# Optimization experiments

Hardware: AMD Instinct MI355X
Metric: run time of the kernel (lower is better)

The kernel has to match this reference:

```python
import jax, jax.numpy as jnp
import numpy as np

N, E = 50000, 800000
NODE_DIM, EDGE_DIM = 128, 32
EGO_H, PEER_H, EDGE_H = 64, 64, 32  # node_hidden=128 split; edge_hidden=32


def setup_inputs() -> dict:
    key = jax.random.key(0)
    ks = jax.random.split(key, 9)
    x = jax.random.normal(ks[0], (N, NODE_DIM), dtype=jnp.float32)
    edge_attrs = jax.random.normal(ks[1], (E, EDGE_DIM), dtype=jnp.float32)
    edge_index = jax.random.randint(ks[2], (2, E), 0, N, dtype=jnp.int32)
    # Linear params (torch convention: W [out, in]), num_layers=1 -> single emb Linear per MLPLayer
    def lin(k, out_d, in_d):
        kw, kb = jax.random.split(k)
        s = 1.0 / np.sqrt(in_d)
        return (jax.random.uniform(kw, (out_d, in_d), minval=-s, maxval=s, dtype=jnp.float32),
                jax.random.uniform(kb, (out_d,), minval=-s, maxval=s, dtype=jnp.float32))
    W_peer, b_peer = lin(ks[3], PEER_H + EDGE_H, NODE_DIM + EDGE_DIM)
    W_ego, b_ego = lin(ks[4], EGO_H, NODE_DIM)
    W_edge, b_edge = lin(ks[5], EDGE_H, EDGE_DIM)
    return {"x": x, "edge_attrs": edge_attrs,
            "W_peer": W_peer, "b_peer": b_peer,
            "W_ego": W_ego, "b_ego": b_ego,
            "W_edge": W_edge, "b_edge": b_edge,
            "edge_index": edge_index}


def reference(x, edge_attrs, W_peer, b_peer, W_ego, b_ego, W_edge, b_edge, edge_index):
    n = x.shape[0]
    # adj_t = SparseTensor(row=ei[0], col=ei[1]).t() -> row = ei[1], col = ei[0]
    row = edge_index[1]
    col = edge_index[0]

    # ego branch
    h_ego = jax.nn.relu(x @ W_ego.T + b_ego)  # [N, EGO_H]

    # degree-based row normalization: deg^-0.5 per adj_t row, inf -> 0
    deg = jax.ops.segment_sum(jnp.ones((row.shape[0],), x.dtype), row, num_segments=n)
    dinv = jnp.where(deg > 0, jax.lax.rsqrt(jnp.maximum(deg, 1.0)) * (deg > 0), 0.0)
    dinv = jnp.where(deg > 0, deg ** -0.5, 0.0)
    norm_val = dinv[row]  # [E]

    # peer branch: gather x[row], cat edge_attrs, linear, normalize, scatter-sum over row
    peer_features = jnp.concatenate([x[row], edge_attrs], axis=1)  # [E, NODE_DIM+EDGE_DIM]
    peer_msg = norm_val[:, None] * (peer_features @ W_peer.T + b_peer)
    h_peer = jax.nn.relu(jax.ops.segment_sum(peer_msg, row, num_segments=n))  # [N, PEER_H+EDGE_H]

    # edge branch
    h_e = jax.nn.relu(edge_attrs @ W_edge.T + b_edge)  # [E, EDGE_H]
    h_e_agg = jax.ops.segment_sum(h_e, row, num_segments=n)  # adj_t.set_value(h_edge).sum(1)
    # norm.matmul(h_edge): out[i] = sum_{e: row[e]==i} norm_val[e] * h_e_agg[col[e]]
    h_e_mm = jax.ops.segment_sum(norm_val[:, None] * h_e_agg[col], row, num_segments=n)
    h_edge = jnp.concatenate([h_e_agg, h_e_mm], axis=1)  # [N, 2*EDGE_H]

    out = jnp.concatenate([h_ego, h_edge, h_peer], axis=1)  # [N, 224]
    return out
```

## Files before the change

### kernel.cpp

```cpp
#include <hip/hip_runtime.h>


typedef float f32x4 __attribute__((ext_vector_type(4)));
typedef short bf16x8 __attribute__((ext_vector_type(8)));

#define BP 256

__device__ __forceinline__ unsigned short f2bf(float f) {
    unsigned u = __float_as_uint(f);
    u += 0x7fffu + ((u >> 16) & 1u);
    return (unsigned short)(u >> 16);
}
__device__ __forceinline__ float bf2f(unsigned short u) {
    return __uint_as_float((unsigned)u << 16);
}
__device__ __forceinline__ ushort4 pk4(float4 v) {
    return (ushort4){f2bf(v.x), f2bf(v.y), f2bf(v.z), f2bf(v.w)};
}
__device__ __forceinline__ bf16x8 pack8(float4 lo, float4 hi) {
    bf16x8 r;
    r[0]=(short)f2bf(lo.x); r[1]=(short)f2bf(lo.y); r[2]=(short)f2bf(lo.z); r[3]=(short)f2bf(lo.w);
    r[4]=(short)f2bf(hi.x); r[5]=(short)f2bf(hi.y); r[6]=(short)f2bf(hi.z); r[7]=(short)f2bf(hi.w);
    return r;
}
__device__ __forceinline__ bf16x8 ld_bfrag(const unsigned short* bp) {
    ushort4 lo = *reinterpret_cast<const ushort4*>(bp);
    ushort4 hi = *reinterpret_cast<const ushort4*>(bp + 16);
    bf16x8 b;
    b[0]=(short)lo.x; b[1]=(short)lo.y; b[2]=(short)lo.z; b[3]=(short)lo.w;
    b[4]=(short)hi.x; b[5]=(short)hi.y; b[6]=(short)hi.z; b[7]=(short)hi.w;
    return b;
}

__global__ __launch_bounds__(256) void k_hist(const int* __restrict__ row,
                                              int* __restrict__ deg, int E) {
    int e = blockIdx.x * blockDim.x + threadIdx.x;
    if (e < E) atomicAdd(&deg[row[e]], 1);
}

__global__ __launch_bounds__(256) void k_scan_partial(const int* __restrict__ deg,
                                                      int* __restrict__ bsum, int N) {
    __shared__ int sh[256];
    int base = blockIdx.x * 1024 + threadIdx.x * 4;
    int s = 0;
#pragma unroll
    for (int q = 0; q < 4; ++q) { int i = base + q; if (i < N) s += deg[i]; }
    sh[threadIdx.x] = s;
    __syncthreads();
    for (int off = 128; off > 0; off >>= 1) {
        if (threadIdx.x < off) sh[threadIdx.x] += sh[threadIdx.x + off];
        __syncthreads();
    }
    if (threadIdx.x == 0) bsum[blockIdx.x] = sh[0];
}

__global__ void k_scan_mid(const int* __restrict__ bsum, int* __restrict__ boff,
                           int* __restrict__ off, int NB, int N) {
    if (threadIdx.x == 0 && blockIdx.x == 0) {
        int acc = 0;
        for (int b = 0; b < NB; ++b) { boff[b] = acc; acc += bsum[b]; }
        off[N] = acc;
    }
}

__global__ __launch_bounds__(256) void k_scan_final(const int* __restrict__ deg,
                                                    const int* __restrict__ boff,
                                                    int* __restrict__ off,
                                                    int* __restrict__ cursor, int N) {
    __shared__ int sh[256];
    int t = threadIdx.x;
    int base = blockIdx.x * 1024 + t * 4;
    int v[4];
#pragma unroll
    for (int q = 0; q < 4; ++q) v[q] = (base + q < N) ? deg[base + q] : 0;
    int ts = v[0] + v[1] + v[2] + v[3];
    sh[t] = ts;
    __syncthreads();
    int incl = ts;
    for (int d = 1; d < 256; d <<= 1) {
        int val = (t >= d) ? sh[t - d] : 0;
        __syncthreads();
        incl += val;
        sh[t] = incl;
        __syncthreads();
    }
    int running = boff[blockIdx.x] + incl - ts;
#pragma unroll
    for (int q = 0; q < 4; ++q) {
        int i = base + q;
        if (i < N) { off[i] = running; cursor[i] = running; running += v[q]; }
    }
}

__global__ __launch_bounds__(256) void k_scatter(const int* __restrict__ row,
                                                 const int* __restrict__ col,
                                                 int* __restrict__ cursor,
                                                 int* __restrict__ eids,
                                                 int* __restrict__ colsort, int E) {
    int e = blockIdx.x * blockDim.x + threadIdx.x;
    if (e >= E) return;
    int pos = atomicAdd(&cursor[row[e]], 1);
    eids[pos] = e;
    colsort[pos] = col[e];
}

__global__ __launch_bounds__(256) void k_prepsd(const int* __restrict__ off,
                                                float* __restrict__ sd,
                                                float* __restrict__ rdeg,
                                                int* __restrict__ nstart, int N) {
    int i = blockIdx.x * blockDim.x + threadIdx.x;
    if (i >= N) return;
    int s = off[i], e = off[i + 1];
    int dg = e - s;
    sd[i]   = dg > 0 ? sqrtf((float)dg) : 0.f;
    rdeg[i] = dg > 0 ? 1.f / (float)dg : 0.f;
    for (int b = (s + BP - 1) / BP; b * BP < e; ++b) nstart[b] = i;
}

__global__ __launch_bounds__(256) void k_prepw(const float* __restrict__ W_ego,
                                               const float* __restrict__ W_peer,
                                               const float* __restrict__ W_edge,
                                               unsigned short* __restrict__ Bt,
                                               unsigned short* __restrict__ Bte) {
    int idx = blockIdx.x * blockDim.x + threadIdx.x;
    if (idx < 160 * 160) {
        int n = idx / 160, k = idx % 160;
        float v;
        if (n < 64) v = (k < 128) ? W_ego[n * 128 + k] : 0.f;
        else        v = W_peer[(n - 64) * 160 + k];
        Bt[idx] = f2bf(v);
    } else if (idx < 160 * 160 + 32 * 32) {
        int j = idx - 160 * 160;
        Bte[j] = f2bf(W_edge[j]);
    }
}

__global__ __launch_bounds__(512) void k_fused(
    const float* __restrict__ ea, const int* __restrict__ eids,
    const int* __restrict__ off, const int* __restrict__ nstart,
    const unsigned short* __restrict__ Bte, const float* __restrict__ b_edge,
    float* __restrict__ eagg, float* __restrict__ sea, int N, int E)
{
    __shared__ unsigned short hs [BP][36];
    __shared__ unsigned short asr[BP][36];
    const int tid  = threadIdx.x;
    const int w    = tid >> 6;
    const int lane = tid & 63;
    const int n16  = lane & 15;
    const int h    = lane >> 4;
    const int P    = blockIdx.x * BP;

    {
        const int tA = w * 32 + n16;
        const int p0 = min(P + tA,      E - 1);
        const int p1 = min(P + tA + 16, E - 1);
        const int e0i = eids[p0];
        const int e1i = eids[p1];
        const float* ap0 = ea + (size_t)e0i * 32 + h * 4;
        const float* ap1 = ea + (size_t)e1i * 32 + h * 4;
        float4 lo0 = *reinterpret_cast<const float4*>(ap0);
        float4 hi0 = *reinterpret_cast<const float4*>(ap0 + 16);
        float4 lo1 = *reinterpret_cast<const float4*>(ap1);
        float4 hi1 = *reinterpret_cast<const float4*>(ap1 + 16);

        *reinterpret_cast<ushort4*>(&asr[tA][h * 4])           = pk4(lo0);
        *reinterpret_cast<ushort4*>(&asr[tA][16 + h * 4])      = pk4(hi0);
        *reinterpret_cast<ushort4*>(&asr[tA + 16][h * 4])      = pk4(lo1);
        *reinterpret_cast<ushort4*>(&asr[tA + 16][16 + h * 4]) = pk4(hi1);

        bf16x8 a0 = pack8(lo0, hi0);
        bf16x8 a1 = pack8(lo1, hi1);
        bf16x8 b0 = ld_bfrag(Bte + (size_t)n16 * 32 + h * 4);
        bf16x8 b1 = ld_bfrag(Bte + (size_t)(16 + n16) * 32 + h * 4);
        f32x4 d00 = {0.f,0.f,0.f,0.f}, d01 = {0.f,0.f,0.f,0.f};
        f32x4 d10 = {0.f,0.f,0.f,0.f}, d11 = {0.f,0.f,0.f,0.f};
        d00 = __builtin_amdgcn_mfma_f32_16x16x32_bf16(a0, b0, d00, 0, 0, 0);
        d01 = __builtin_amdgcn_mfma_f32_16x16x32_bf16(a0, b1, d01, 0, 0, 0);
        d10 = __builtin_amdgcn_mfma_f32_16x16x32_bf16(a1, b0, d10, 0, 0, 0);
        d11 = __builtin_amdgcn_mfma_f32_16x16x32_bf16(a1, b1, d11, 0, 0, 0);

        const int tr0 = w * 32 + h * 4;
        float be0 = b_edge[n16], be1 = b_edge[16 + n16];
#pragma unroll
        for (int r = 0; r < 4; ++r) {
            hs[tr0 + r][n16]           = f2bf(fmaxf(d00[r] + be0, 0.f));
            hs[tr0 + r][16 + n16]      = f2bf(fmaxf(d01[r] + be1, 0.f));
            hs[tr0 + 16 + r][n16]      = f2bf(fmaxf(d10[r] + be0, 0.f));
            hs[tr0 + 16 + r][16 + n16] = f2bf(fmaxf(d11[r] + be1, 0.f));
        }
    }
    __syncthreads();

    const int c = lane & 7, sub = lane >> 3;
    const int node0 = nstart[blockIdx.x];

    for (int n = node0 + w; n < N; n += 8) {
        int s0 = off[n];
        if (s0 >= P + BP) break;
        int e0 = off[n + 1];
        int s = max(s0, P) - P, eEnd = min(e0, P + BP) - P;
        float4 hv = {0.f,0.f,0.f,0.f}, av = {0.f,0.f,0.f,0.f};
        for (int t = s + sub; t < eEnd; t += 8) {
            ushort4 uh = *reinterpret_cast<const ushort4*>(&hs [t][c * 4]);
            ushort4 ua = *reinterpret_cast<const ushort4*>(&asr[t][c * 4]);
            hv.x += bf2f(uh.x); hv.y += bf2f(uh.y); hv.z += bf2f(uh.z); hv.w += bf2f(uh.w);
            av.x += bf2f(ua.x); av.y += bf2f(ua.y); av.z += bf2f(ua.z); av.w += bf2f(ua.w);
        }
#pragma unroll
        for (int m = 8; m < 64; m <<= 1) {
            hv.x += __shfl_xor(hv.x, m); hv.y += __shfl_xor(hv.y, m);
            hv.z += __shfl_xor(hv.z, m); hv.w += __shfl_xor(hv.w, m);
            av.x += __shfl_xor(av.x, m); av.y += __shfl_xor(av.y, m);
            av.z += __shfl_xor(av.z, m); av.w += __shfl_xor(av.w, m);
        }
        if (lane < 8) {
            float* pe = eagg + (size_t)n * 32 + c * 4;
            float* ps = sea  + (size_t)n * 32 + c * 4;
            bool interior = (s0 >= P) && (e0 <= P + BP);
            if (interior) {
                *reinterpret_cast<float4*>(pe) = hv;
                *reinterpret_cast<float4*>(ps) = av;
            } else {
                atomicAdd(pe+0,hv.x); atomicAdd(pe+1,hv.y);
                atomicAdd(pe+2,hv.z); atomicAdd(pe+3,hv.w);
                atomicAdd(ps+0,av.x); atomicAdd(ps+1,av.y);
                atomicAdd(ps+2,av.z); atomicAdd(ps+3,av.w);
            }
        }
    }
}

__global__ __launch_bounds__(256) void k_mmagg(
    const int* __restrict__ colsort, const int* __restrict__ off,
    const float* __restrict__ eagg, float* __restrict__ out, int N)
{
    int wid  = (blockIdx.x * blockDim.x + threadIdx.x) >> 6;
    int lane = threadIdx.x & 63;
    if (wid >= N) return;
    int s = off[wid], e = off[wid + 1];
    int c   = lane & 7;
    int sub = lane >> 3;
    float4 acc = {0.f, 0.f, 0.f, 0.f};
    float4 acc2 = {0.f, 0.f, 0.f, 0.f};
    for (int t0 = s; t0 < e; t0 += 16) {
        int t1 = t0 + sub, t2 = t0 + 8 + sub;
        if (t1 < e) {
            float4 v = reinterpret_cast<const float4*>(eagg + (size_t)colsort[t1] * 32)[c];
            acc.x += v.x; acc.y += v.y; acc.z += v.z; acc.w += v.w;
        }
        if (t2 < e) {
            float4 v = reinterpret_cast<const float4*>(eagg + (size_t)colsort[t2] * 32)[c];
            acc2.x += v.x; acc2.y += v.y; acc2.z += v.z; acc2.w += v.w;
        }
    }
    acc.x += acc2.x; acc.y += acc2.y; acc.z += acc2.z; acc.w += acc2.w;
#pragma unroll
    for (int m = 8; m < 64; m <<= 1) {
        acc.x += __shfl_xor(acc.x, m);
        acc.y += __shfl_xor(acc.y, m);
        acc.z += __shfl_xor(acc.z, m);
        acc.w += __shfl_xor(acc.w, m);
    }
    int dg = e - s;
    float dinv = dg > 0 ? rsqrtf((float)dg) : 0.f;
    if (lane < 8) {
        float4 o4 = {acc.x * dinv, acc.y * dinv, acc.z * dinv, acc.w * dinv};
        reinterpret_cast<float4*>(out + (size_t)wid * 224 + 96)[c] = o4;
        float4 eg = reinterpret_cast<const float4*>(eagg + (size_t)wid * 32)[c];
        reinterpret_cast<float4*>(out + (size_t)wid * 224 + 64)[c] = eg;
    }
}

__global__ __launch_bounds__(256) void k_node3(
    const float* __restrict__ x, const float* __restrict__ sea,
    const float* __restrict__ sd, const float* __restrict__ rdeg,
    const unsigned short* __restrict__ Bt,
    const float* __restrict__ b_ego, const float* __restrict__ b_peer,
    float* __restrict__ out, int N)
{
    const int lane = threadIdx.x & 63;
    const int wv   = threadIdx.x >> 6;
    const int wm   = blockIdx.x * 64 + wv * 16;
    const int n16  = lane & 15;
    const int h    = lane >> 4;

    const int m_l = min(wm + n16, N - 1);

    f32x4 acc[10];
#pragma unroll
    for (int f = 0; f < 10; ++f) acc[f] = (f32x4){0.f,0.f,0.f,0.f};

#pragma unroll
    for (int kc = 0; kc < 5; ++kc) {
        bf16x8 bfr[10];
#pragma unroll
        for (int f = 0; f < 10; ++f)
            bfr[f] = ld_bfrag(Bt + (size_t)(f * 16 + n16) * 160 + kc * 32 + h * 4);
        float4 lo, hi;
        if (kc < 4) {
            const float* ap = x + (size_t)m_l * 128 + kc * 32 + h * 4;
            lo = *reinterpret_cast<const float4*>(ap);
            hi = *reinterpret_cast<const float4*>(ap + 16);
        } else {
            float r = rdeg[m_l];
            const float* ap = sea + (size_t)m_l * 32 + h * 4;
            lo = *reinterpret_cast<const float4*>(ap);
            hi = *reinterpret_cast<const float4*>(ap + 16);
            lo.x*=r; lo.y*=r; lo.z*=r; lo.w*=r;
            hi.x*=r; hi.y*=r; hi.z*=r; hi.w*=r;
        }
        bf16x8 a = pack8(lo, hi);
#pragma unroll
        for (int f = 0; f < 10; ++f)
            acc[f] = __builtin_amdgcn_mfma_f32_16x16x32_bf16(a, bfr[f], acc[f], 0, 0, 0);
    }

    const int r4 = h * 4;
    float sdv[4];
#pragma unroll
    for (int r = 0; r < 4; ++r) {
        int node = wm + r4 + r;
        sdv[r] = (node < N) ? sd[node] : 0.f;
    }
#pragma unroll
    for (int f = 0; f < 10; ++f) {
        int c = f * 16 + n16;
        float be = (c < 64)  ? b_ego[c] : 0.f;
        float bp = (c >= 64) ? b_peer[c - 64] : 0.f;
#pragma unroll
        for (int r = 0; r < 4; ++r) {
            int node = wm + r4 + r;
            if (node >= N) continue;
            float v = acc[f][r];
            if (c < 64)
                out[(size_t)node * 224 + c] = fmaxf(v + be, 0.f);
            else
                out[(size_t)node * 224 + 64 + c] = fmaxf(sdv[r] * (v + bp), 0.f);
        }
    }
}

extern "C" void kernel_launch(void* const* d_in, const int* in_sizes, int n_in,
                              void* d_out, int out_size, void* d_ws, size_t ws_size,
                              hipStream_t stream)
{
    const float* x      = (const float*)d_in[0];
    const float* ea     = (const float*)d_in[1];
    const float* W_peer = (const float*)d_in[2];
    const float* b_peer = (const float*)d_in[3];
    const float* W_ego  = (const float*)d_in[4];
    const float* b_ego  = (const float*)d_in[5];
    const float* W_edge = (const float*)d_in[6];
    const float* b_edge = (const float*)d_in[7];
    const int*   ei     = (const int*)d_in[8];

    const int N = in_sizes[0] / 128;
    const int E = in_sizes[8] / 2;
    const int* col = ei;
    const int* row = ei + E;
    const int nblocks = (E + BP - 1) / BP;

    int*   deg_i   = (int*)d_ws;
    float* eagg    = (float*)(deg_i + N);
    float* sea     = eagg + (size_t)32 * N;
    int*   off     = (int*)(sea + (size_t)32 * N);
    int*   cursor  = off + (N + 1);
    int*   bsum    = cursor + N;
    int*   boff    = bsum + 64;
    int*   eids    = boff + 64;
    int*   colsort = eids + E;
    float* sd      = (float*)(colsort + E);
    float* rdeg    = sd + N;
    int*   nstart  = (int*)(rdeg + N);
    unsigned short* Bt  = (unsigned short*)(nstart + nblocks);
    unsigned short* Bte = Bt + 160 * 160;
    float* out     = (float*)d_out;

    hipMemsetAsync(d_ws, 0, (size_t)(65 * N) * sizeof(int), stream);

    const int TB = 256;
    const int NB = (N + 1023) / 1024;
    k_hist        <<<(E + TB - 1) / TB, TB, 0, stream>>>(row, deg_i, E);
    k_prepw       <<<(160*160 + 32*32 + TB - 1) / TB, TB, 0, stream>>>(W_ego, W_peer, W_edge, Bt, Bte);
    k_scan_partial<<<NB, TB, 0, stream>>>(deg_i, bsum, N);
    k_scan_mid    <<<1, 64, 0, stream>>>(bsum, boff, off, NB, N);
    k_scan_final  <<<NB, TB, 0, stream>>>(deg_i, boff, off, cursor, N);
    k_prepsd      <<<(N + TB - 1) / TB, TB, 0, stream>>>(off, sd, rdeg, nstart, N);
    k_scatter     <<<(E + TB - 1) / TB, TB, 0, stream>>>(row, col, cursor, eids, colsort, E);

    k_fused<<<nblocks, 512, 0, stream>>>(ea, eids, off, nstart, Bte, b_edge,
                                         eagg, sea, N, E);

    const int agg_grid = (N + 3) / 4;
    k_mmagg<<<agg_grid, TB, 0, stream>>>(colsort, off, eagg, out, N);
    k_node3<<<(N + 63) / 64, TB, 0, stream>>>(x, sea, sd, rdeg, Bt,
                                              b_ego, b_peer, out, N);
}
```

Before: 215.4 us.

## Fold prepsd and selective zeroing into scan, pack edge ids and cols

The per-node degree prep (sqrt, reciprocal, block-start table) moves into the final scan kernel, which removes one launch. The full workspace memset is replaced by a small degree-zeroing kernel. The eagg and sea rows are now cleared only for nodes with no edges or whose edge range crosses a block boundary, relying on the fused kernel to fully write the other rows. Edge ids and column indices are interleaved into one int2 array so the scatter does a single 8-byte store, at the cost of wider loads in the consumers that need only one field.

```diff
diff --git a/kernel.cpp b/kernel.cpp
--- a/kernel.cpp
+++ b/kernel.cpp
@@ -32,6 +32,11 @@
     return b;
 }
 
+__global__ __launch_bounds__(256) void k_zero(int* __restrict__ deg, int N) {
+    int i = blockIdx.x * blockDim.x + threadIdx.x;
+    if (i < N) deg[i] = 0;
+}
+
 __global__ __launch_bounds__(256) void k_hist(const int* __restrict__ row,
                                               int* __restrict__ deg, int E) {
     int e = blockIdx.x * blockDim.x + threadIdx.x;
@@ -63,10 +68,12 @@
     }
 }
 
-__global__ __launch_bounds__(256) void k_scan_final(const int* __restrict__ deg,
-                                                    const int* __restrict__ boff,
-                                                    int* __restrict__ off,
-                                                    int* __restrict__ cursor, int N) {
+__global__ __launch_bounds__(256) void k_scan_final(
+    const int* __restrict__ deg, const int* __restrict__ boff,
+    int* __restrict__ off, int* __restrict__ cursor,
+    float* __restrict__ sd, float* __restrict__ rdeg, int* __restrict__ nstart,
+    float* __restrict__ eagg, float* __restrict__ sea, int N)
+{
     __shared__ int sh[256];
     int t = threadIdx.x;
     int base = blockIdx.x * 1024 + t * 4;
@@ -88,33 +95,34 @@
 #pragma unroll
     for (int q = 0; q < 4; ++q) {
         int i = base + q;
-        if (i < N) { off[i] = running; cursor[i] = running; running += v[q]; }
+        if (i < N) {
+            int s = running, e = running + v[q];
+            off[i] = s; cursor[i] = s;
+            int dg = v[q];
+            sd[i]   = dg > 0 ? sqrtf((float)dg) : 0.f;
+            rdeg[i] = dg > 0 ? 1.f / (float)dg : 0.f;
+            for (int b = (s + BP - 1) / BP; b * BP < e; ++b) nstart[b] = i;
+            bool zneed = (dg == 0) || ((s / BP) != ((e - 1) / BP));
+            if (zneed) {
+                float4 z = {0.f, 0.f, 0.f, 0.f};
+                float4* pe = reinterpret_cast<float4*>(eagg + (size_t)i * 32);
+                float4* ps = reinterpret_cast<float4*>(sea  + (size_t)i * 32);
+#pragma unroll
+                for (int q2 = 0; q2 < 8; ++q2) { pe[q2] = z; ps[q2] = z; }
+            }
+            running = e;
+        }
     }
 }
 
 __global__ __launch_bounds__(256) void k_scatter(const int* __restrict__ row,
                                                  const int* __restrict__ col,
                                                  int* __restrict__ cursor,
-                                                 int* __restrict__ eids,
-                                                 int* __restrict__ colsort, int E) {
+                                                 int2* __restrict__ edat, int E) {
     int e = blockIdx.x * blockDim.x + threadIdx.x;
     if (e >= E) return;
     int pos = atomicAdd(&cursor[row[e]], 1);
-    eids[pos] = e;
-    colsort[pos] = col[e];
-}
-
-__global__ __launch_bounds__(256) void k_prepsd(const int* __restrict__ off,
-                                                float* __restrict__ sd,
-                                                float* __restrict__ rdeg,
-                                                int* __restrict__ nstart, int N) {
-    int i = blockIdx.x * blockDim.x + threadIdx.x;
-    if (i >= N) return;
-    int s = off[i], e = off[i + 1];
-    int dg = e - s;
-    sd[i]   = dg > 0 ? sqrtf((float)dg) : 0.f;
-    rdeg[i] = dg > 0 ? 1.f / (float)dg : 0.f;
-    for (int b = (s + BP - 1) / BP; b * BP < e; ++b) nstart[b] = i;
+    edat[pos] = make_int2(e, col[e]);
 }
 
 __global__ __launch_bounds__(256) void k_prepw(const float* __restrict__ W_ego,
@@ -136,7 +144,7 @@
 }
 
 __global__ __launch_bounds__(512) void k_fused(
-    const float* __restrict__ ea, const int* __restrict__ eids,
+    const float* __restrict__ ea, const int2* __restrict__ edat,
     const int* __restrict__ off, const int* __restrict__ nstart,
     const unsigned short* __restrict__ Bte, const float* __restrict__ b_edge,
     float* __restrict__ eagg, float* __restrict__ sea, int N, int E)
@@ -154,8 +162,8 @@
         const int tA = w * 32 + n16;
         const int p0 = min(P + tA,      E - 1);
         const int p1 = min(P + tA + 16, E - 1);
-        const int e0i = eids[p0];
-        const int e1i = eids[p1];
+        const int e0i = edat[p0].x;
+        const int e1i = edat[p1].x;
         const float* ap0 = ea + (size_t)e0i * 32 + h * 4;
         const float* ap1 = ea + (size_t)e1i * 32 + h * 4;
         float4 lo0 = *reinterpret_cast<const float4*>(ap0);
@@ -231,7 +239,7 @@
 }
 
 __global__ __launch_bounds__(256) void k_mmagg(
-    const int* __restrict__ colsort, const int* __restrict__ off,
+    const int2* __restrict__ edat, const int* __restrict__ off,
     const float* __restrict__ eagg, float* __restrict__ out, int N)
 {
     int wid  = (blockIdx.x * blockDim.x + threadIdx.x) >> 6;
@@ -245,11 +253,11 @@
     for (int t0 = s; t0 < e; t0 += 16) {
         int t1 = t0 + sub, t2 = t0 + 8 + sub;
         if (t1 < e) {
-            float4 v = reinterpret_cast<const float4*>(eagg + (size_t)colsort[t1] * 32)[c];
+            float4 v = reinterpret_cast<const float4*>(eagg + (size_t)edat[t1].y * 32)[c];
             acc.x += v.x; acc.y += v.y; acc.z += v.z; acc.w += v.w;
         }
         if (t2 < e) {
-            float4 v = reinterpret_cast<const float4*>(eagg + (size_t)colsort[t2] * 32)[c];
+            float4 v = reinterpret_cast<const float4*>(eagg + (size_t)edat[t2].y * 32)[c];
             acc2.x += v.x; acc2.y += v.y; acc2.z += v.z; acc2.w += v.w;
         }
     }
@@ -360,39 +368,37 @@
     const int* row = ei + E;
     const int nblocks = (E + BP - 1) / BP;
 
-    int*   deg_i   = (int*)d_ws;
+    int2*  edat    = (int2*)d_ws;
+    int*   deg_i   = (int*)(edat + E);
     float* eagg    = (float*)(deg_i + N);
     float* sea     = eagg + (size_t)32 * N;
     int*   off     = (int*)(sea + (size_t)32 * N);
     int*   cursor  = off + (N + 1);
     int*   bsum    = cursor + N;
     int*   boff    = bsum + 64;
-    int*   eids    = boff + 64;
-    int*   colsort = eids + E;
-    float* sd      = (float*)(colsort + E);
+    float* sd      = (float*)(boff + 64);
     float* rdeg    = sd + N;
     int*   nstart  = (int*)(rdeg + N);
     unsigned short* Bt  = (unsigned short*)(nstart + nblocks);
     unsigned short* Bte = Bt + 160 * 160;
     float* out     = (float*)d_out;
 
-    hipMemsetAsync(d_ws, 0, (size_t)(65 * N) * sizeof(int), stream);
-
     const int TB = 256;
     const int NB = (N + 1023) / 1024;
+    k_zero        <<<(N + TB - 1) / TB, TB, 0, stream>>>(deg_i, N);
+    k_prepw       <<<(160*160 + 32*32 + TB - 1) / TB, TB, 0, stream>>>(W_ego, W_peer, W_edge, Bt, Bte);
     k_hist        <<<(E + TB - 1) / TB, TB, 0, stream>>>(row, deg_i, E);
-    k_prepw       <<<(160*160 + 32*32 + TB - 1) / TB, TB, 0, stream>>>(W_ego, W_peer, W_edge, Bt, Bte);
     k_scan_partial<<<NB, TB, 0, stream>>>(deg_i, bsum, N);
     k_scan_mid    <<<1, 64, 0, stream>>>(bsum, boff, off, NB, N);
-    k_scan_final  <<<NB, TB, 0, stream>>>(deg_i, boff, off, cursor, N);
-    k_prepsd      <<<(N + TB - 1) / TB, TB, 0, stream>>>(off, sd, rdeg, nstart, N);
-    k_scatter     <<<(E + TB - 1) / TB, TB, 0, stream>>>(row, col, cursor, eids, colsort, E);
-
-    k_fused<<<nblocks, 512, 0, stream>>>(ea, eids, off, nstart, Bte, b_edge,
+    k_scan_final  <<<NB, TB, 0, stream>>>(deg_i, boff, off, cursor, sd, rdeg,
+                                          nstart, eagg, sea, N);
+    k_scatter     <<<(E + TB - 1) / TB, TB, 0, stream>>>(row, col, cursor, edat, E);
+
+    k_fused<<<nblocks, 512, 0, stream>>>(ea, edat, off, nstart, Bte, b_edge,
                                          eagg, sea, N, E);
 
     const int agg_grid = (N + 3) / 4;
-    k_mmagg<<<agg_grid, TB, 0, stream>>>(colsort, off, eagg, out, N);
+    k_mmagg<<<agg_grid, TB, 0, stream>>>(edat, off, eagg, out, N);
     k_node3<<<(N + 63) / 64, TB, 0, stream>>>(x, sea, sd, rdeg, Bt,
                                               b_ego, b_peer, out, N);
 }
```

Measured after the change: 212.5 us. About the same (-1.4%).
